# Optimization experiments

Hardware: AMD Instinct MI355X
Metric: run time of the kernel (lower is better)

## Reference

```python
import jax, jax.numpy as jnp
import numpy as np

B, T, E, A = 4, 4096, 1024, 1024

def setup_inputs() -> dict:
    key = jax.random.key(0)
    k1, k2, k3, k4 = jax.random.split(key, 4)
    scale = 1.0 / np.sqrt(E)  # ~ nn.Linear default init scale
    return {
        "embedded": jax.random.normal(k1, (B, T, E), dtype=jnp.float32),
        "Wq": jax.random.uniform(k2, (A, E), jnp.float32, -scale, scale),
        "Wk": jax.random.uniform(k3, (A, E), jnp.float32, -scale, scale),
        "Wv": jax.random.uniform(k4, (A, E), jnp.float32, -scale, scale),
    }

def reference(embedded, Wq, Wk, Wv):
    # QKV projections (nn.Linear without bias: x @ W.T)
    q = jnp.einsum('bte,ae->bta', embedded, Wq)
    k = jnp.einsum('bte,ae->bta', embedded, Wk)
    v = jnp.einsum('bte,ae->bta', embedded, Wv)
    A_dim = q.shape[-1]
    # scaled scores [B, T, T]
    scores = jnp.einsum('bqa,bka->bqk', q, k) / jnp.sqrt(jnp.float32(A_dim))
    # causal mask (lower triangular allowed)
    Tq = scores.shape[-1]
    causal = jnp.tril(jnp.ones((Tq, Tq), dtype=bool))
    scores = jnp.where(causal, scores, -jnp.inf)
    probs = jax.nn.softmax(scores, axis=-1)
    out = jnp.einsum('bqk,bka->bqa', probs, v)
    return jnp.round(out, 4)
```

## Files before the change

kernel.cpp:

```cpp
#include <hip/hip_runtime.h>
#include <hip/hip_bf16.h>

using bf16 = __hip_bfloat16;

typedef __attribute__((ext_vector_type(4))) float f32x4;
typedef __attribute__((ext_vector_type(8))) short short8;

typedef const void __attribute__((address_space(1)))* gas1_t;
typedef void __attribute__((address_space(3)))* las3_t;
#define GLDS(gp, lp) __builtin_amdgcn_global_load_lds((gas1_t)(gp), (las3_t)(lp), 16, 0, 0)

__device__ inline short f2bfbits(float f) {
  union { bf16 h; short s; } u;
  u.h = __float2bfloat16(f);
  return u.s;
}
__device__ inline float bf2f(short u) {
  unsigned x = ((unsigned)(unsigned short)u) << 16;
  float f; __builtin_memcpy(&f, &x, 4); return f;
}

__device__ inline void store_out(float* C, size_t idx, float v) { C[idx] = v; }
__device__ inline void store_out(bf16* C, size_t idx, float v) { C[idx] = __float2bfloat16(v); }

template<typename TOUT, int MODE>
__global__ __launch_bounds__(512, 2) void gemm256(
    const short* __restrict__ A, int lda, size_t sAz,
    const short* __restrict__ B, int ldb, size_t sBz,
    TOUT* __restrict__ C, int ldc, size_t sCz,
    int K, float scale)
{
  int bx, by;
  if constexpr (MODE == 1) {
    const int i = blockIdx.x;
    by = (int)((__builtin_sqrtf(8.f * (float)i + 1.f) - 1.f) * 0.5f);
    if (((by * (by + 1)) >> 1) > i) by--;
    else if ((((by + 1) * (by + 2)) >> 1) <= i) by++;
    bx = i - ((by * (by + 1)) >> 1);
  } else {
    bx = blockIdx.x; by = blockIdx.y;
  }
  const int z = blockIdx.z;
  const int tri_by = (by * (by + 1)) >> 1;

  A += (size_t)z * sAz;
  B += (size_t)z * sBz;
  C += (size_t)z * sCz;

  int Klen = K;
  if (MODE == 2) Klen = min(K, (by + 1) * 256);
  const int NT = Klen >> 5;

  __shared__ short As[3][256 * 32];
  __shared__ short Bs[3][256 * 32];

  const int t = threadIdx.x;
  const int lane = t & 63;
  const int wave = t >> 6;
  const int wm = wave >> 2;
  const int wn = wave & 3;
  const int fr = lane & 15, kh = lane >> 4;
  const int koff = ((kh ^ ((fr >> 1) & 3)) << 3);

  int srow[2], scol[2];
  #pragma unroll
  for (int j = 0; j < 2; j++) {
    int e = j * 512 + t;
    srow[j] = e >> 2;
    scol[j] = (((e & 3) ^ ((e >> 3) & 3)) << 3);
  }

  f32x4 acc[8][4];
  #pragma unroll
  for (int i = 0; i < 8; i++)
    #pragma unroll
    for (int j = 0; j < 4; j++) acc[i][j] = (f32x4){0.f, 0.f, 0.f, 0.f};

  auto STAGE_A = [&](int kt) {
    const int buf = kt % 3, k0 = kt * 32;
    #pragma unroll
    for (int j = 0; j < 2; j++) {
      const short* pa;
      if constexpr (MODE == 2)
        pa = A + (size_t)(tri_by + (k0 >> 8)) * 65536 + (size_t)srow[j] * 256 + (k0 & 255) + scol[j];
      else
        pa = A + (size_t)(by * 256 + srow[j]) * lda + k0 + scol[j];
      GLDS(pa, (char*)&As[buf][0] + j * 8192 + wave * 1024);
    }
  };
  auto STAGE_B = [&](int kt) {
    const int buf = kt % 3, k0 = kt * 32;
    #pragma unroll
    for (int j = 0; j < 2; j++) {
      const short* pb = B + (size_t)(bx * 256 + srow[j]) * ldb + k0 + scol[j];
      GLDS(pb, (char*)&Bs[buf][0] + j * 8192 + wave * 1024);
    }
  };

  STAGE_A(0); STAGE_B(0);
  STAGE_A(1); STAGE_B(1);
  asm volatile("s_waitcnt vmcnt(4)\ns_barrier" ::: "memory");

  const int arow = wm * 128 + fr;
  const int brow = wn * 64 + fr;

  for (int kt = 0; kt < NT; kt++) {
    const short* as = &As[kt % 3][0];
    const short* bs = &Bs[kt % 3][0];
    short8 af[4], bfr[4];

    #pragma unroll
    for (int n = 0; n < 4; n++) bfr[n] = *(const short8*)&bs[(brow + n * 16) * 32 + koff];
    #pragma unroll
    for (int m = 0; m < 4; m++) af[m] = *(const short8*)&as[(arow + m * 16) * 32 + koff];
    if (kt + 2 < NT) STAGE_A(kt + 2);
    __builtin_amdgcn_s_barrier();
    asm volatile("s_waitcnt lgkmcnt(0)" ::: "memory");
    __builtin_amdgcn_sched_barrier(0);
    __builtin_amdgcn_s_setprio(1);
    #pragma unroll
    for (int m = 0; m < 4; m++)
      #pragma unroll
      for (int n = 0; n < 4; n++)
        acc[m][n] = __builtin_amdgcn_mfma_f32_16x16x32_bf16(af[m], bfr[n], acc[m][n], 0, 0, 0);
    __builtin_amdgcn_s_setprio(0);
    __builtin_amdgcn_sched_barrier(0);

    #pragma unroll
    for (int m = 0; m < 4; m++) af[m] = *(const short8*)&as[(arow + (m + 4) * 16) * 32 + koff];
    if (kt + 2 < NT) STAGE_B(kt + 2);
    __builtin_amdgcn_s_barrier();
    asm volatile("s_waitcnt lgkmcnt(0)" ::: "memory");
    __builtin_amdgcn_sched_barrier(0);
    __builtin_amdgcn_s_setprio(1);
    #pragma unroll
    for (int m = 0; m < 4; m++)
      #pragma unroll
      for (int n = 0; n < 4; n++)
        acc[m + 4][n] = __builtin_amdgcn_mfma_f32_16x16x32_bf16(af[m], bfr[n], acc[m + 4][n], 0, 0, 0);
    __builtin_amdgcn_s_setprio(0);
    __builtin_amdgcn_sched_barrier(0);

    if (kt + 2 < NT)      asm volatile("s_waitcnt vmcnt(4)\ns_barrier" ::: "memory");
    else if (kt + 1 < NT) asm volatile("s_waitcnt vmcnt(0)\ns_barrier" ::: "memory");
  }

  #pragma unroll
  for (int m = 0; m < 8; m++)
    #pragma unroll
    for (int n = 0; n < 4; n++) {
      int col_l = wn * 64 + n * 16 + fr;
      #pragma unroll
      for (int r = 0; r < 4; r++) {
        int row_l = wm * 128 + m * 16 + kh * 4 + r;
        if constexpr (MODE == 1)
          store_out(C, (size_t)(tri_by + bx) * 65536 + (size_t)row_l * 256 + col_l,
                    acc[m][n][r] * scale);
        else
          store_out(C, (size_t)(by * 256 + row_l) * ldc + bx * 256 + col_l,
                    acc[m][n][r] * scale);
      }
    }
}

__global__ __launch_bounds__(256) void gemm128(
    const short* __restrict__ A, int lda,
    const short* __restrict__ B, int ldb,
    bf16* __restrict__ C, int ldc, int K, float scale)
{
  const int bx = blockIdx.x, by = blockIdx.y;
  __shared__ short a_lds[128 * 32];
  __shared__ short b_lds[128 * 32];

  const int t = threadIdx.x;
  const int lane = t & 63;
  const int wave = t >> 6;
  const int wm = wave >> 1, wn = wave & 1;
  const int fr = lane & 15, kh = lane >> 4;

  f32x4 acc[4][4];
  #pragma unroll
  for (int i = 0; i < 4; i++)
    #pragma unroll
    for (int j = 0; j < 4; j++) acc[i][j] = (f32x4){0.f, 0.f, 0.f, 0.f};

  for (int k0 = 0; k0 < K; k0 += 32) {
    #pragma unroll
    for (int i = 0; i < 2; i++) {
      int e = i * 256 + t;
      int r_ = e >> 2, c_ = (e & 3) * 8;
      GLDS(A + (size_t)(by * 128 + r_) * lda + k0 + c_, (char*)a_lds + i * 4096 + wave * 1024);
      GLDS(B + (size_t)(bx * 128 + r_) * ldb + k0 + c_, (char*)b_lds + i * 4096 + wave * 1024);
    }
    __syncthreads();

    short8 af[4], bfr[4];
    #pragma unroll
    for (int m = 0; m < 4; m++)
      af[m] = *(const short8*)&a_lds[(wm * 64 + m * 16 + fr) * 32 + kh * 8];
    #pragma unroll
    for (int n = 0; n < 4; n++)
      bfr[n] = *(const short8*)&b_lds[(wn * 64 + n * 16 + fr) * 32 + kh * 8];
    #pragma unroll
    for (int m = 0; m < 4; m++)
      #pragma unroll
      for (int n = 0; n < 4; n++)
        acc[m][n] = __builtin_amdgcn_mfma_f32_16x16x32_bf16(af[m], bfr[n], acc[m][n], 0, 0, 0);
    __syncthreads();
  }

  #pragma unroll
  for (int m = 0; m < 4; m++)
    #pragma unroll
    for (int n = 0; n < 4; n++) {
      int col = bx * 128 + wn * 64 + n * 16 + fr;
      #pragma unroll
      for (int r = 0; r < 4; r++) {
        int row = by * 128 + wm * 64 + m * 16 + kh * 4 + r;
        C[(size_t)row * ldc + col] = __float2bfloat16(acc[m][n][r] * scale);
      }
    }
}

__global__ __launch_bounds__(256) void cvt_bf16(
    const float* __restrict__ in, bf16* __restrict__ out, int n, float scale)
{
  for (int i = (blockIdx.x * 256 + threadIdx.x) * 8; i < n; i += gridDim.x * 2048) {
    f32x4 v0 = *(const f32x4*)&in[i];
    f32x4 v1 = *(const f32x4*)&in[i + 4];
    short8 o = { f2bfbits(v0[0] * scale), f2bfbits(v0[1] * scale),
                 f2bfbits(v0[2] * scale), f2bfbits(v0[3] * scale),
                 f2bfbits(v1[0] * scale), f2bfbits(v1[1] * scale),
                 f2bfbits(v1[2] * scale), f2bfbits(v1[3] * scale) };
    *(short8*)&out[i] = o;
  }
}

__global__ __launch_bounds__(256) void cvt_t_bf16(
    const float* __restrict__ in, bf16* __restrict__ out, int N)
{
  __shared__ float tile[64][65];
  const int bx = blockIdx.x, by = blockIdx.y;
  const int t = threadIdx.x;
  #pragma unroll
  for (int i = 0; i < 16; i++) {
    int e = i * 256 + t;
    int r = e >> 6, c = e & 63;
    tile[r][c] = in[(size_t)(by * 64 + r) * N + bx * 64 + c];
  }
  __syncthreads();
  #pragma unroll
  for (int i = 0; i < 16; i++) {
    int e = i * 256 + t;
    int r = e >> 6, c = e & 63;
    out[(size_t)(bx * 64 + r) * N + by * 64 + c] = __float2bfloat16(tile[c][r]);
  }
}

__global__ __launch_bounds__(256) void softmax_causal_packed(short* SP, int T)
{
  __shared__ float rowv[4096];
  __shared__ float red[4];
  const int r = blockIdx.x;
  const int z = blockIdx.y;
  const int rb = r >> 8, rl = r & 255;
  const size_t tri = (size_t)((rb * (rb + 1)) >> 1);
  short* base = SP + (size_t)z * 136 * 65536;
  const int L = r + 1;
  const int kend = (rb + 1) * 256;
  const int t = threadIdx.x;

  float lmax = -3.0e38f;
  for (int i = t * 8; i < kend; i += 2048) {
    short8 s = *(const short8*)(base + (tri + (i >> 8)) * 65536 + (size_t)rl * 256 + (i & 255));
    #pragma unroll
    for (int j = 0; j < 8; j++) {
      float v = bf2f(s[j]);
      rowv[i + j] = v;
      if (i + j < L) lmax = fmaxf(lmax, v);
    }
  }
  #pragma unroll
  for (int o = 32; o > 0; o >>= 1) lmax = fmaxf(lmax, __shfl_down(lmax, o));
  if ((t & 63) == 0) red[t >> 6] = lmax;
  __syncthreads();
  const float m = fmaxf(fmaxf(red[0], red[1]), fmaxf(red[2], red[3]));
  __syncthreads();

  float lsum = 0.f;
  for (int i = t; i < kend; i += 256) {
    float e = (i < L) ? __expf(rowv[i] - m) : 0.f;
    rowv[i] = e;
    lsum += e;
  }
  #pragma unroll
  for (int o = 32; o > 0; o >>= 1) lsum += __shfl_down(lsum, o);
  if ((t & 63) == 0) red[t >> 6] = lsum;
  __syncthreads();
  const float inv = 1.f / (red[0] + red[1] + red[2] + red[3]);

  for (int i = t * 8; i < kend; i += 2048) {
    short8 o;
    #pragma unroll
    for (int j = 0; j < 8; j++) o[j] = f2bfbits(rowv[i + j] * inv);
    *(short8*)(base + (tri + (i >> 8)) * 65536 + (size_t)rl * 256 + (i & 255)) = o;
  }
}

extern "C" void kernel_launch(void* const* d_in, const int* in_sizes, int n_in,
                              void* d_out, int out_size, void* d_ws, size_t ws_size,
                              hipStream_t stream) {
  (void)in_sizes; (void)n_in; (void)out_size; (void)ws_size;
  const float* X  = (const float*)d_in[0];
  const float* Wq = (const float*)d_in[1];
  const float* Wk = (const float*)d_in[2];
  const float* Wv = (const float*)d_in[3];
  float* Out = (float*)d_out;

  const int Bn = 4, T = 4096, E = 1024, Ad = 1024;
  const int M = Bn * T;

  char* ws = (char*)d_ws;
  short* Q2  = (short*)ws;
  short* Vt  = (short*)(ws + 33554432);
  short* Xb  = (short*)(ws + 67108864);
  short* WqT = (short*)(ws + 100663296);
  short* WkT = (short*)(ws + 102760448);
  short* Wvb = (short*)(ws + 104857600);
  short* W2T = (short*)(ws + 106954752);
  short* SP  = (short*)(ws + 109051904);

  dim3 blk(256), blk5(512);
  const size_t SPz = (size_t)136 * 65536;

  cvt_bf16<<<dim3(8192), blk, 0, stream>>>(X, (bf16*)Xb, M * E, 1.0f);
  cvt_t_bf16<<<dim3(16, 16), blk, 0, stream>>>(Wq, (bf16*)WqT, E);
  cvt_t_bf16<<<dim3(16, 16), blk, 0, stream>>>(Wk, (bf16*)WkT, E);
  cvt_bf16<<<dim3(512), blk, 0, stream>>>(Wv, (bf16*)Wvb, Ad * E, 1.0f);

  gemm128<<<dim3(8, 8), blk, 0, stream>>>(
      WkT, Ad, WqT, Ad, (bf16*)W2T, E, Ad, 0.03125f);

  gemm256<bf16, 0><<<dim3(1024 / 256, M / 256), blk5, 0, stream>>>(
      Xb, E, 0, W2T, E, 0, (bf16*)Q2, 1024, 0, E, 1.0f);

  gemm256<bf16, 0><<<dim3(M / 256, Ad / 256), blk5, 0, stream>>>(
      Wvb, E, 0, Xb, E, 0, (bf16*)Vt, M, 0, E, 1.0f);

  gemm256<bf16, 1><<<dim3(136, 1, Bn), blk5, 0, stream>>>(
      Q2, 1024, (size_t)T * 1024,
      Xb, 1024, (size_t)T * 1024,
      (bf16*)SP, 256, SPz, E, 1.0f);

  softmax_causal_packed<<<dim3(T, Bn), blk, 0, stream>>>(SP, T);

  gemm256<float, 2><<<dim3(Ad / 256, T / 256, Bn), blk5, 0, stream>>>(
      SP, 256, SPz,
      Vt, M, (size_t)T,
      Out, Ad, (size_t)T * Ad, T, 1.0f);
}
```

Before: 384.1 us.

## Add dedicated PV GEMM kernel with 256x128 tiles and load-balanced causal scheduling

Replaces the generic MODE 2 path of gemm256 for the probs·V product with a specialized gemm_pv kernel. It uses 256x128 output tiles, double-buffered LDS and launch bounds allowing two blocks per CU, which gives 512 blocks instead of 256. The block order pairs short and long causal row blocks (g and 15-g) to even out load across the triangular work. The price is smaller N tiles, so each A tile is reused less, plus hardcoded shapes and strides.

Result: no change. 384.4 us (+0.1%).

```diff
diff --git a/kernel.cpp b/kernel.cpp
--- a/kernel.cpp
+++ b/kernel.cpp
@@ -47,9 +47,7 @@
   B += (size_t)z * sBz;
   C += (size_t)z * sCz;
 
-  int Klen = K;
-  if (MODE == 2) Klen = min(K, (by + 1) * 256);
-  const int NT = Klen >> 5;
+  const int NT = K >> 5;
 
   __shared__ short As[3][256 * 32];
   __shared__ short Bs[3][256 * 32];
@@ -80,11 +78,7 @@
     const int buf = kt % 3, k0 = kt * 32;
     #pragma unroll
     for (int j = 0; j < 2; j++) {
-      const short* pa;
-      if constexpr (MODE == 2)
-        pa = A + (size_t)(tri_by + (k0 >> 8)) * 65536 + (size_t)srow[j] * 256 + (k0 & 255) + scol[j];
-      else
-        pa = A + (size_t)(by * 256 + srow[j]) * lda + k0 + scol[j];
+      const short* pa = A + (size_t)(by * 256 + srow[j]) * lda + k0 + scol[j];
       GLDS(pa, (char*)&As[buf][0] + j * 8192 + wave * 1024);
     }
   };
@@ -159,6 +153,122 @@
         else
           store_out(C, (size_t)(by * 256 + row_l) * ldc + bx * 256 + col_l,
                     acc[m][n][r] * scale);
+      }
+    }
+}
+
+__global__ __launch_bounds__(256, 2) void gemm_pv(
+    const short* __restrict__ SP, const short* __restrict__ Vt,
+    float* __restrict__ Out)
+{
+  const int w = blockIdx.x;
+  const int k = w >> 8, c = w & 255;
+  const int bx = c & 7;
+  const int g = (c >> 3) & 7;
+  const int z = c >> 6;
+  const int by = k ? 15 - g : g;
+  const int tri_by = (by * (by + 1)) >> 1;
+
+  const short* A = SP + (size_t)z * 136 * 65536;
+  const int Klen = (by + 1) * 256;
+  const int NT = Klen >> 5;
+
+  __shared__ short As[2][256 * 32];
+  __shared__ short Bs[2][128 * 32];
+
+  const int t = threadIdx.x;
+  const int lane = t & 63;
+  const int wave = t >> 6;
+  const int wm = wave >> 1;
+  const int wn = wave & 1;
+  const int fr = lane & 15, kh = lane >> 4;
+  const int koff = ((kh ^ ((fr >> 1) & 3)) << 3);
+
+  f32x4 acc[8][4];
+  #pragma unroll
+  for (int i = 0; i < 8; i++)
+    #pragma unroll
+    for (int j = 0; j < 4; j++) acc[i][j] = (f32x4){0.f, 0.f, 0.f, 0.f};
+
+  auto STAGE_A = [&](int kt) {
+    const int buf = kt & 1, k0 = kt * 32;
+    #pragma unroll
+    for (int j = 0; j < 4; j++) {
+      int e = j * 256 + t;
+      int row = e >> 2;
+      int sc = (((e & 3) ^ ((row >> 1) & 3)) << 3);
+      const short* pa = A + (size_t)(tri_by + (k0 >> 8)) * 65536
+                          + (size_t)row * 256 + (k0 & 255) + sc;
+      GLDS(pa, (char*)&As[buf][0] + j * 4096 + wave * 1024);
+    }
+  };
+  auto STAGE_B = [&](int kt) {
+    const int buf = kt & 1, k0 = kt * 32;
+    #pragma unroll
+    for (int j = 0; j < 2; j++) {
+      int e = j * 256 + t;
+      int row = e >> 2;
+      int sc = (((e & 3) ^ ((row >> 1) & 3)) << 3);
+      const short* pb = Vt + (size_t)(bx * 128 + row) * 16384 + z * 4096 + k0 + sc;
+      GLDS(pb, (char*)&Bs[buf][0] + j * 4096 + wave * 1024);
+    }
+  };
+
+  STAGE_A(0); STAGE_B(0);
+  asm volatile("s_waitcnt vmcnt(0)\ns_barrier" ::: "memory");
+
+  const int arow = wm * 128 + fr;
+  const int brow = wn * 64 + fr;
+
+  for (int kt = 0; kt < NT; kt++) {
+    const short* as = &As[kt & 1][0];
+    const short* bs = &Bs[kt & 1][0];
+    short8 af[4], bfr[4];
+
+    #pragma unroll
+    for (int n = 0; n < 4; n++) bfr[n] = *(const short8*)&bs[(brow + n * 16) * 32 + koff];
+    #pragma unroll
+    for (int m = 0; m < 4; m++) af[m] = *(const short8*)&as[(arow + m * 16) * 32 + koff];
+    if (kt + 1 < NT) STAGE_A(kt + 1);
+    asm volatile("s_waitcnt lgkmcnt(0)" ::: "memory");
+    __builtin_amdgcn_sched_barrier(0);
+    __builtin_amdgcn_s_setprio(1);
+    #pragma unroll
+    for (int m = 0; m < 4; m++)
+      #pragma unroll
+      for (int n = 0; n < 4; n++)
+        acc[m][n] = __builtin_amdgcn_mfma_f32_16x16x32_bf16(af[m], bfr[n], acc[m][n], 0, 0, 0);
+    __builtin_amdgcn_s_setprio(0);
+    __builtin_amdgcn_sched_barrier(0);
+
+    #pragma unroll
+    for (int m = 0; m < 4; m++) af[m] = *(const short8*)&as[(arow + (m + 4) * 16) * 32 + koff];
+    if (kt + 1 < NT) STAGE_B(kt + 1);
+    asm volatile("s_waitcnt lgkmcnt(0)" ::: "memory");
+    __builtin_amdgcn_sched_barrier(0);
+    __builtin_amdgcn_s_setprio(1);
+    #pragma unroll
+    for (int m = 0; m < 4; m++)
+      #pragma unroll
+      for (int n = 0; n < 4; n++)
+        acc[m + 4][n] = __builtin_amdgcn_mfma_f32_16x16x32_bf16(af[m], bfr[n], acc[m + 4][n], 0, 0, 0);
+    __builtin_amdgcn_s_setprio(0);
+    __builtin_amdgcn_sched_barrier(0);
+
+    if (kt + 1 < NT)
+      asm volatile("s_waitcnt vmcnt(0)\ns_barrier" ::: "memory");
+  }
+
+  float* Cz = Out + (size_t)z * 4096 * 1024;
+  #pragma unroll
+  for (int m = 0; m < 8; m++)
+    #pragma unroll
+    for (int n = 0; n < 4; n++) {
+      int col = bx * 128 + wn * 64 + n * 16 + fr;
+      #pragma unroll
+      for (int r = 0; r < 4; r++) {
+        int row_l = wm * 128 + m * 16 + kh * 4 + r;
+        Cz[(size_t)(by * 256 + row_l) * 1024 + col] = acc[m][n][r];
       }
     }
 }
@@ -354,8 +464,5 @@
 
   softmax_causal_packed<<<dim3(T, Bn), blk, 0, stream>>>(SP, T);
 
-  gemm256<float, 2><<<dim3(Ad / 256, T / 256, Bn), blk5, 0, stream>>>(
-      SP, 256, SPz,
-      Vt, M, (size_t)T,
-      Out, Ad, (size_t)T * Ad, T, 1.0f);
-}
+  gemm_pv<<<dim3(512), blk, 0, stream>>>(SP, Vt, Out);
+}
```
